# Performance work log

Measured on AMD Instinct MI355X. Metric: run time of the kernel, lower is better.

## Reference

```python
import jax, jax.numpy as jnp
import numpy as np

B, T, C, H = 4, 4096, 1024, 64

def setup_inputs() -> dict:
    key = jax.random.key(0)
    kx, kq, kk, kv = jax.random.split(key, 4)
    # nn.Linear weights are [out, in]; we store them that way and use einsum.
    s = 1.0 / np.sqrt(C)
    return {
        "x": jax.random.normal(kx, (B, T, C), dtype=jnp.float32),
        "Wq": jax.random.uniform(kq, (H, C), dtype=jnp.float32, minval=-s, maxval=s),
        "Wk": jax.random.uniform(kk, (H, C), dtype=jnp.float32, minval=-s, maxval=s),
        "Wv": jax.random.uniform(kv, (H, C), dtype=jnp.float32, minval=-s, maxval=s),
    }

def reference(x, Wq, Wk, Wv):
    # x: [B, T, C]; W*: [H, C] (torch Linear layout)
    Q = jnp.einsum('btc,hc->bth', x, Wq)  # [B, T, H]
    K = jnp.einsum('btc,hc->bth', x, Wk)
    V = jnp.einsum('btc,hc->bth', x, Wv)
    scale = K.shape[-1] ** -0.5
    scores = jnp.einsum('bqh,bkh->bqk', Q, K) * scale  # [B, T, T]
    Tn = x.shape[1]
    causal = jnp.tril(jnp.ones((Tn, Tn), dtype=bool))
    scores = jnp.where(causal, scores, -jnp.inf)
    attn = jax.nn.softmax(scores, axis=-1)
    return jnp.einsum('bqk,bkh->bqh', attn, V)  # [B, T, H]
```

## Files before the change

### kernel.cpp

```cpp
#include <hip/hip_runtime.h>
#include <hip/hip_bf16.h>

#define B_ 4
#define T_ 4096
#define C_ 1024
#define H_ 64

typedef __bf16 bf16x8 __attribute__((ext_vector_type(8)));
typedef float f32x4 __attribute__((ext_vector_type(4)));
typedef unsigned short u16x8 __attribute__((ext_vector_type(8)));

union Frag8 { uint4 u; bf16x8 b; u16x8 s; };

__device__ inline unsigned short bfbits(float f) {
  union { __hip_bfloat16 h; unsigned short u; } cv;
  cv.h = __float2bfloat16(f);
  return cv.u;
}

__device__ inline float b2f(unsigned u) {
  union { unsigned i; float f; } c; c.i = u << 16; return c.f;
}

__device__ inline bf16x8 ldb8(const unsigned short* p) {
  Frag8 f; f.u = *(const uint4*)p; return f.b;
}

__device__ inline unsigned pkbf(float a, float b) {
  union { float f; unsigned u; } ua, ub; ua.f = a; ub.f = b;
  return __builtin_amdgcn_perm(ub.u + 0x8000u, ua.u + 0x8000u, 0x07060302u);
}

__device__ inline Frag8 packA(float4 a0, float4 a1) {
  Frag8 af;
  af.s[0] = bfbits(a0.x); af.s[1] = bfbits(a0.y);
  af.s[2] = bfbits(a0.z); af.s[3] = bfbits(a0.w);
  af.s[4] = bfbits(a1.x); af.s[5] = bfbits(a1.y);
  af.s[6] = bfbits(a1.z); af.s[7] = bfbits(a1.w);
  return af;
}

__device__ inline void gload16(const void* g, void* l) {
  __builtin_amdgcn_global_load_lds(
      (const __attribute__((address_space(1))) unsigned int*)g,
      (__attribute__((address_space(3))) unsigned int*)l, 16, 0, 0);
}

__global__ __launch_bounds__(256) void wconv(const float* __restrict__ Wq,
                                             const float* __restrict__ Wk,
                                             const float* __restrict__ Wv,
                                             unsigned short* __restrict__ Wb) {
  int i = blockIdx.x * 256 + threadIdx.x;
  size_t e = (size_t)i * 4;
  const float* src = (e < 65536) ? (Wq + e)
                   : (e < 131072 ? (Wk + (e - 65536)) : (Wv + (e - 131072)));
  float4 v = *(const float4*)src;
  unsigned long long o =
      (unsigned long long)bfbits(v.x)
    | ((unsigned long long)bfbits(v.y) << 16)
    | ((unsigned long long)bfbits(v.z) << 32)
    | ((unsigned long long)bfbits(v.w) << 48);
  *(unsigned long long*)(Wb + e) = o;
}

__global__ __launch_bounds__(256) void qkv_proj(const float* __restrict__ x,
                                                const unsigned short* __restrict__ Wb,
                                                unsigned short* __restrict__ qkv,
                                                unsigned short* __restrict__ Vt) {
  __shared__ float xs[2][2048];
  __shared__ unsigned short Wsh[2][12288];
  const int lane = threadIdx.x & 63;
  const int wave = threadIdx.x >> 6;
  const int q16 = lane & 15, quad = lane >> 4;
  const int x7 = q16 & 7;
  const size_t row0 = (size_t)blockIdx.x * 32;

  const int sr = lane >> 4;
  const int sc_pos = lane & 15;
  const int rloc = lane >> 3;
  const int cpos = lane & 7;

  f32x4 acc[2][3] = {};

  auto stage = [&](int buf, int kc) {
#pragma unroll
    for (int ii = 0; ii < 2; ++ii) {
      int i = wave * 2 + ii;
      int r = i * 4 + sr;
      int sg = (sc_pos >> 1) ^ (r & 7);
      const float* gp = x + (row0 + r) * C_ + kc + sg * 8 + (sc_pos & 1) * 4;
      gload16(gp, &xs[buf][i * 256]);
    }
#pragma unroll
    for (int jj = 0; jj < 6; ++jj) {
      int j = wave * 6 + jj;
      int g = j * 8 + rloc;
      const unsigned short* gp = Wb + (size_t)(g >> 6) * 65536
                                    + (size_t)(g & 63) * C_ + kc + (cpos ^ rloc) * 8;
      gload16(gp, &Wsh[buf][j * 512]);
    }
  };

  stage(0, 0);
  __syncthreads();

  int cur = 0;
  for (int t = 0; t < 16; ++t) {
    if (t < 15) stage(cur ^ 1, (t + 1) * 64);
    const float* Xc = xs[cur];
    const unsigned short* Wc = Wsh[cur];
#pragma unroll
    for (int s = 0; s < 2; ++s) {
      bf16x8 bf[3];
#pragma unroll
      for (int ct = 0; ct < 3; ++ct) {
        int g = wave * 48 + ct * 16 + q16;
        bf[ct] = ldb8(&Wc[g * 64 + (((s * 4 + quad) ^ x7) * 8)]);
      }
#pragma unroll
      for (int rt = 0; rt < 2; ++rt) {
        int r = rt * 16 + q16;
        int p = ((s * 4 + quad) ^ (r & 7)) * 8;
        const float* ap = &Xc[r * 64 + p];
        float4 a0 = *(const float4*)ap;
        float4 a1 = *(const float4*)(ap + 4);
        Frag8 af = packA(a0, a1);
#pragma unroll
        for (int ct = 0; ct < 3; ++ct)
          acc[rt][ct] = __builtin_amdgcn_mfma_f32_16x16x32_bf16(
              af.b, bf[ct], acc[rt][ct], 0, 0, 0);
      }
    }
    __syncthreads();
    cur ^= 1;
  }

  const int bb = (int)(blockIdx.x >> 7);
#pragma unroll
  for (int rt = 0; rt < 2; ++rt) {
    const int t0 = (int)(row0 - (size_t)bb * T_) + rt * 16 + quad * 4;
#pragma unroll
    for (int ct = 0; ct < 3; ++ct) {
      int gcol = wave * 48 + ct * 16;
      int mat = gcol >> 6, h = (gcol & 63) + q16;
      if (mat == 2) {
        ushort4 v;
        v.x = bfbits(acc[rt][ct][0]); v.y = bfbits(acc[rt][ct][1]);
        v.z = bfbits(acc[rt][ct][2]); v.w = bfbits(acc[rt][ct][3]);
        *(ushort4*)(Vt + ((size_t)bb * H_ + h) * T_ + t0) = v;
      } else {
        float scale = (mat == 0) ? 0.18033688f : 1.0f;
#pragma unroll
        for (int r = 0; r < 4; ++r) {
          size_t row = row0 + rt * 16 + quad * 4 + r;
          qkv[(size_t)mat * 1048576 + row * H_ + h] = bfbits(acc[rt][ct][r] * scale);
        }
      }
    }
  }
}

__global__ __launch_bounds__(256) void attn(const unsigned short* __restrict__ Q,
                                            const unsigned short* __restrict__ K,
                                            const unsigned short* __restrict__ Vt,
                                            float* __restrict__ part,
                                            int lgch, int nslots) {
  const int b = blockIdx.x >> 6;
  const int qblk = 63 - (blockIdx.x & 63);
  const int ki = qblk + 1;
  const int c = blockIdx.y;
  const int cst = c << lgch;
  if (cst >= ki) return;
  const int tcnt = 1 << lgch;
  const int kend = (ki < cst + tcnt) ? ki : cst + tcnt;

  __shared__ unsigned short Ks[2][4096];
  __shared__ unsigned short Vs[2][4096];
  const int lane = threadIdx.x & 63;
  const int wave = threadIdx.x >> 6;
  const int q16 = lane & 15, quad = lane >> 4;
  const int x7 = q16 & 7;
  const int rloc = lane >> 3, cpos = lane & 7;

  const unsigned short* Qb = Q + (size_t)b * T_ * H_;
  const unsigned short* Kb = K + (size_t)b * T_ * H_;
  const unsigned short* Vtb = Vt + (size_t)b * H_ * T_;

  int psi_[2];
#pragma unroll
  for (int ii = 0; ii < 2; ++ii) {
    int g = (wave * 2 + ii) * 8 + rloc;
    psi_[ii] = 8 * ((g & 15) >> 2) + (g & 3) + 4 * ((g >> 4) & 1) + 32 * (g >> 5);
  }

  auto stage = [&](int buf, int kt) {
    const int kkb = kt * 64;
#pragma unroll
    for (int ii = 0; ii < 2; ++ii) {
      int i = wave * 2 + ii;
      gload16(Kb + (size_t)(kkb + psi_[ii]) * H_ + (cpos ^ rloc) * 8,
              &Ks[buf][i * 512]);
      gload16(Vtb + (size_t)(i * 8 + rloc) * T_ + kkb + (cpos ^ rloc) * 8,
              &Vs[buf][i * 512]);
    }
  };

  const int q0w = qblk * 64 + wave * 16;
  bf16x8 qf0 = ldb8(Qb + (size_t)(q0w + q16) * H_ + quad * 8);
  bf16x8 qf1 = ldb8(Qb + (size_t)(q0w + q16) * H_ + 32 + quad * 8);

  f32x4 o[4] = {};
  float m = -3.0e38f, l = 0.0f;
  const int q_abs = q0w + q16;

  stage(0, cst);
  __syncthreads();

  int cur = 0;
  for (int kt = cst; kt < kend; ++kt) {
    const int kkb = kt * 64;
    if (kt + 1 < kend) stage(cur ^ 1, kt + 1);
    const unsigned short* Kc = Ks[cur];
    const unsigned short* Vc = Vs[cur];

    f32x4 st[4];
#pragma unroll
    for (int kb = 0; kb < 4; ++kb) {
      bf16x8 ka0 = ldb8(&Kc[(kb * 16 + q16) * 64 + ((quad ^ x7) * 8)]);
      bf16x8 ka1 = ldb8(&Kc[(kb * 16 + q16) * 64 + (((quad + 4) ^ x7) * 8)]);
      f32x4 s = {0.f, 0.f, 0.f, 0.f};
      s = __builtin_amdgcn_mfma_f32_16x16x32_bf16(ka0, qf0, s, 0, 0, 0);
      s = __builtin_amdgcn_mfma_f32_16x16x32_bf16(ka1, qf1, s, 0, 0, 0);
      st[kb] = s;
    }
    if (kt == ki - 1) {
      const int kb8q = kkb + 8 * quad;
#pragma unroll
      for (int kb = 0; kb < 4; ++kb) {
        const int kof = kb8q + 4 * (kb & 1) + 32 * (kb >> 1);
#pragma unroll
        for (int r = 0; r < 4; ++r)
          if (kof + r > q_abs) st[kb][r] = -3.0e38f;
      }
    }

    float mloc = fmaxf(fmaxf(st[0][0], st[0][1]), fmaxf(st[0][2], st[0][3]));
#pragma unroll
    for (int kb = 1; kb < 4; ++kb)
      mloc = fmaxf(mloc, fmaxf(fmaxf(st[kb][0], st[kb][1]), fmaxf(st[kb][2], st[kb][3])));
    mloc = fmaxf(mloc, __shfl_xor(mloc, 16));
    mloc = fmaxf(mloc, __shfl_xor(mloc, 32));
    const bool defer = __all(mloc - m <= 8.0f);
    const float mnew = defer ? m : fmaxf(m, mloc);
    float lsum = 0.f;
    unsigned pk[4][2];
#pragma unroll
    for (int kb = 0; kb < 4; ++kb) {
      float p0 = exp2f(st[kb][0] - mnew);
      float p1 = exp2f(st[kb][1] - mnew);
      float p2 = exp2f(st[kb][2] - mnew);
      float p3 = exp2f(st[kb][3] - mnew);
      lsum += (p0 + p1) + (p2 + p3);
      pk[kb][0] = pkbf(p0, p1);
      pk[kb][1] = pkbf(p2, p3);
    }
    if (defer) {
      l += lsum;
    } else {
      float alpha = exp2f(m - mnew);
      l = l * alpha + lsum;
      m = mnew;
#pragma unroll
      for (int ct = 0; ct < 4; ++ct) {
        o[ct][0] *= alpha; o[ct][1] *= alpha;
        o[ct][2] *= alpha; o[ct][3] *= alpha;
      }
    }

#pragma unroll
    for (int ks = 0; ks < 2; ++ks) {
      Frag8 pf;
      pf.u.x = pk[2 * ks][0];
      pf.u.y = pk[2 * ks][1];
      pf.u.z = pk[2 * ks + 1][0];
      pf.u.w = pk[2 * ks + 1][1];
      int vp = ((ks * 4 + quad) ^ x7) * 8;
      bf16x8 v0 = ldb8(&Vc[(q16 + 0)  * 64 + vp]);
      bf16x8 v1 = ldb8(&Vc[(q16 + 16) * 64 + vp]);
      bf16x8 v2 = ldb8(&Vc[(q16 + 32) * 64 + vp]);
      bf16x8 v3 = ldb8(&Vc[(q16 + 48) * 64 + vp]);
      o[0] = __builtin_amdgcn_mfma_f32_16x16x32_bf16(v0, pf.b, o[0], 0, 0, 0);
      o[1] = __builtin_amdgcn_mfma_f32_16x16x32_bf16(v1, pf.b, o[1], 0, 0, 0);
      o[2] = __builtin_amdgcn_mfma_f32_16x16x32_bf16(v2, pf.b, o[2], 0, 0, 0);
      o[3] = __builtin_amdgcn_mfma_f32_16x16x32_bf16(v3, pf.b, o[3], 0, 0, 0);
    }
    __syncthreads();
    cur ^= 1;
  }

  const int qtl = qblk * 4 + wave;
  float lr = l;
  lr += __shfl_xor(lr, 16);
  lr += __shfl_xor(lr, 32);
  float* Pf = part + ((size_t)((b << 8) + qtl) * nslots + c) * 544;
  unsigned* Pw = (unsigned*)Pf;
#pragma unroll
  for (int ct = 0; ct < 4; ++ct) {
    uint2 w;
    w.x = pkbf(o[ct][0], o[ct][1]);
    w.y = pkbf(o[ct][2], o[ct][3]);
    *(uint2*)&Pw[(ct * 64 + lane) * 2] = w;
  }
  if (quad == 0) { Pf[512 + q16] = m; Pf[528 + q16] = lr; }
}

__global__ __launch_bounds__(256) void attn_merge(const float* __restrict__ part,
                                                  float* __restrict__ out,
                                                  int lgch, int nslots) {
  const int qt = blockIdx.x;
  const int qtl = qt & 255, b = qt >> 8;
  const int ki = (qtl >> 2) + 1;
  const int nch = (ki + (1 << lgch) - 1) >> lgch;
  const int t = threadIdx.x;
  const int row = t >> 4;
  const int col0 = (t & 15) * 4;
  const int ct = col0 >> 4;
  const int quad_s = (col0 >> 2) & 3;
  const int lane0 = quad_s * 16 + row;
  const float* P0 = part + (size_t)qt * nslots * 544;
  float M = -3.0e38f;
  for (int c2 = 0; c2 < nch; ++c2) M = fmaxf(M, P0[c2 * 544 + 512 + row]);
  float L = 0.f;
  float ax = 0.f, ay = 0.f, az = 0.f, aw = 0.f;
  for (int c2 = 0; c2 < nch; ++c2) {
    const float* P = P0 + c2 * 544;
    float wgt = exp2f(P[512 + row] - M);
    L += wgt * P[528 + row];
    const unsigned* Pww = (const unsigned*)P;
    uint2 wd = *(const uint2*)&Pww[(ct * 64 + lane0) * 2];
    ax += wgt * b2f(wd.x & 0xffffu);
    ay += wgt * b2f(wd.x >> 16);
    az += wgt * b2f(wd.y & 0xffffu);
    aw += wgt * b2f(wd.y >> 16);
  }
  float inv = 1.0f / L;
  float4 r = {ax * inv, ay * inv, az * inv, aw * inv};
  *(float4*)(out + ((size_t)b * T_ + qtl * 16 + row) * H_ + col0) = r;
}

extern "C" void kernel_launch(void* const* d_in, const int* in_sizes, int n_in,
                              void* d_out, int out_size, void* d_ws, size_t ws_size,
                              hipStream_t stream) {
  const float* x  = (const float*)d_in[0];
  const float* Wq = (const float*)d_in[1];
  const float* Wk = (const float*)d_in[2];
  const float* Wv = (const float*)d_in[3];
  float* out = (float*)d_out;
  unsigned short* ws = (unsigned short*)d_ws;

  unsigned short* Wb  = ws;
  unsigned short* qkv = ws + 196608;
  unsigned short* Vt  = qkv + (size_t)2 * 1048576;
  float* part = (float*)(ws + 196608 + (size_t)3 * 1048576);

  const size_t base_bytes = ((size_t)196608 + (size_t)3 * 1048576) * 2;
  const size_t need16 = base_bytes + (size_t)1024 * 16 * 544 * 4;
  int lgch = 3, ny = 8, nslots = 8;
  if (ws_size >= need16) { lgch = 2; ny = 16; nslots = 16; }

  wconv<<<192, 256, 0, stream>>>(Wq, Wk, Wv, Wb);
  qkv_proj<<<512, 256, 0, stream>>>(x, Wb, qkv, Vt);
  attn<<<dim3(256, ny), 256, 0, stream>>>(qkv, qkv + 1048576, Vt, part, lgch, nslots);
  attn_merge<<<1024, 256, 0, stream>>>(part, out, lgch, nslots);
}
```

Before: 161.8 us.

## Widen attention blocks to 128 queries so K/V tiles are shared by eight waves

```diff
diff --git a/kernel.cpp b/kernel.cpp
--- a/kernel.cpp
+++ b/kernel.cpp
@@ -160,19 +160,19 @@
   }
 }
 
-__global__ __launch_bounds__(256) void attn(const unsigned short* __restrict__ Q,
+__global__ __launch_bounds__(512) void attn(const unsigned short* __restrict__ Q,
                                             const unsigned short* __restrict__ K,
                                             const unsigned short* __restrict__ Vt,
                                             float* __restrict__ part,
                                             int lgch, int nslots) {
-  const int b = blockIdx.x >> 6;
-  const int qblk = 63 - (blockIdx.x & 63);
-  const int ki = qblk + 1;
+  const int b = blockIdx.x >> 5;
+  const int qblk = 31 - (blockIdx.x & 31);
+  const int ki_block = 2 * qblk + 2;
   const int c = blockIdx.y;
   const int cst = c << lgch;
-  if (cst >= ki) return;
+  if (cst >= ki_block) return;
   const int tcnt = 1 << lgch;
-  const int kend = (ki < cst + tcnt) ? ki : cst + tcnt;
+  const int kend = (ki_block < cst + tcnt) ? ki_block : cst + tcnt;
 
   __shared__ unsigned short Ks[2][4096];
   __shared__ unsigned short Vs[2][4096];
@@ -186,26 +186,20 @@
   const unsigned short* Kb = K + (size_t)b * T_ * H_;
   const unsigned short* Vtb = Vt + (size_t)b * H_ * T_;
 
-  int psi_[2];
-#pragma unroll
-  for (int ii = 0; ii < 2; ++ii) {
-    int g = (wave * 2 + ii) * 8 + rloc;
-    psi_[ii] = 8 * ((g & 15) >> 2) + (g & 3) + 4 * ((g >> 4) & 1) + 32 * (g >> 5);
-  }
+  const int g_ = wave * 8 + rloc;
+  const int psi_ = 8 * ((g_ & 15) >> 2) + (g_ & 3) + 4 * ((g_ >> 4) & 1)
+                 + 32 * (g_ >> 5);
 
   auto stage = [&](int buf, int kt) {
     const int kkb = kt * 64;
-#pragma unroll
-    for (int ii = 0; ii < 2; ++ii) {
-      int i = wave * 2 + ii;
-      gload16(Kb + (size_t)(kkb + psi_[ii]) * H_ + (cpos ^ rloc) * 8,
-              &Ks[buf][i * 512]);
-      gload16(Vtb + (size_t)(i * 8 + rloc) * T_ + kkb + (cpos ^ rloc) * 8,
-              &Vs[buf][i * 512]);
-    }
+    gload16(Kb + (size_t)(kkb + psi_) * H_ + (cpos ^ rloc) * 8,
+            &Ks[buf][wave * 512]);
+    gload16(Vtb + (size_t)(wave * 8 + rloc) * T_ + kkb + (cpos ^ rloc) * 8,
+            &Vs[buf][wave * 512]);
   };
 
-  const int q0w = qblk * 64 + wave * 16;
+  const int q0w = qblk * 128 + wave * 16;
+  const int kiW = 2 * qblk + (wave >> 2) + 1;
   bf16x8 qf0 = ldb8(Qb + (size_t)(q0w + q16) * H_ + quad * 8);
   bf16x8 qf1 = ldb8(Qb + (size_t)(q0w + q16) * H_ + 32 + quad * 8);
 
@@ -220,98 +214,103 @@
   for (int kt = cst; kt < kend; ++kt) {
     const int kkb = kt * 64;
     if (kt + 1 < kend) stage(cur ^ 1, kt + 1);
-    const unsigned short* Kc = Ks[cur];
-    const unsigned short* Vc = Vs[cur];
-
-    f32x4 st[4];
-#pragma unroll
-    for (int kb = 0; kb < 4; ++kb) {
-      bf16x8 ka0 = ldb8(&Kc[(kb * 16 + q16) * 64 + ((quad ^ x7) * 8)]);
-      bf16x8 ka1 = ldb8(&Kc[(kb * 16 + q16) * 64 + (((quad + 4) ^ x7) * 8)]);
-      f32x4 s = {0.f, 0.f, 0.f, 0.f};
-      s = __builtin_amdgcn_mfma_f32_16x16x32_bf16(ka0, qf0, s, 0, 0, 0);
-      s = __builtin_amdgcn_mfma_f32_16x16x32_bf16(ka1, qf1, s, 0, 0, 0);
-      st[kb] = s;
-    }
-    if (kt == ki - 1) {
-      const int kb8q = kkb + 8 * quad;
+    if (kt < kiW) {
+      const unsigned short* Kc = Ks[cur];
+      const unsigned short* Vc = Vs[cur];
+
+      f32x4 st[4];
 #pragma unroll
       for (int kb = 0; kb < 4; ++kb) {
-        const int kof = kb8q + 4 * (kb & 1) + 32 * (kb >> 1);
-#pragma unroll
-        for (int r = 0; r < 4; ++r)
-          if (kof + r > q_abs) st[kb][r] = -3.0e38f;
-      }
-    }
-
-    float mloc = fmaxf(fmaxf(st[0][0], st[0][1]), fmaxf(st[0][2], st[0][3]));
-#pragma unroll
-    for (int kb = 1; kb < 4; ++kb)
-      mloc = fmaxf(mloc, fmaxf(fmaxf(st[kb][0], st[kb][1]), fmaxf(st[kb][2], st[kb][3])));
-    mloc = fmaxf(mloc, __shfl_xor(mloc, 16));
-    mloc = fmaxf(mloc, __shfl_xor(mloc, 32));
-    const bool defer = __all(mloc - m <= 8.0f);
-    const float mnew = defer ? m : fmaxf(m, mloc);
-    float lsum = 0.f;
-    unsigned pk[4][2];
-#pragma unroll
-    for (int kb = 0; kb < 4; ++kb) {
-      float p0 = exp2f(st[kb][0] - mnew);
-      float p1 = exp2f(st[kb][1] - mnew);
-      float p2 = exp2f(st[kb][2] - mnew);
-      float p3 = exp2f(st[kb][3] - mnew);
-      lsum += (p0 + p1) + (p2 + p3);
-      pk[kb][0] = pkbf(p0, p1);
-      pk[kb][1] = pkbf(p2, p3);
-    }
-    if (defer) {
-      l += lsum;
-    } else {
-      float alpha = exp2f(m - mnew);
-      l = l * alpha + lsum;
-      m = mnew;
-#pragma unroll
-      for (int ct = 0; ct < 4; ++ct) {
-        o[ct][0] *= alpha; o[ct][1] *= alpha;
-        o[ct][2] *= alpha; o[ct][3] *= alpha;
-      }
-    }
-
-#pragma unroll
-    for (int ks = 0; ks < 2; ++ks) {
-      Frag8 pf;
-      pf.u.x = pk[2 * ks][0];
-      pf.u.y = pk[2 * ks][1];
-      pf.u.z = pk[2 * ks + 1][0];
-      pf.u.w = pk[2 * ks + 1][1];
-      int vp = ((ks * 4 + quad) ^ x7) * 8;
-      bf16x8 v0 = ldb8(&Vc[(q16 + 0)  * 64 + vp]);
-      bf16x8 v1 = ldb8(&Vc[(q16 + 16) * 64 + vp]);
-      bf16x8 v2 = ldb8(&Vc[(q16 + 32) * 64 + vp]);
-      bf16x8 v3 = ldb8(&Vc[(q16 + 48) * 64 + vp]);
-      o[0] = __builtin_amdgcn_mfma_f32_16x16x32_bf16(v0, pf.b, o[0], 0, 0, 0);
-      o[1] = __builtin_amdgcn_mfma_f32_16x16x32_bf16(v1, pf.b, o[1], 0, 0, 0);
-      o[2] = __builtin_amdgcn_mfma_f32_16x16x32_bf16(v2, pf.b, o[2], 0, 0, 0);
-      o[3] = __builtin_amdgcn_mfma_f32_16x16x32_bf16(v3, pf.b, o[3], 0, 0, 0);
+        bf16x8 ka0 = ldb8(&Kc[(kb * 16 + q16) * 64 + ((quad ^ x7) * 8)]);
+        bf16x8 ka1 = ldb8(&Kc[(kb * 16 + q16) * 64 + (((quad + 4) ^ x7) * 8)]);
+        f32x4 s = {0.f, 0.f, 0.f, 0.f};
+        s = __builtin_amdgcn_mfma_f32_16x16x32_bf16(ka0, qf0, s, 0, 0, 0);
+        s = __builtin_amdgcn_mfma_f32_16x16x32_bf16(ka1, qf1, s, 0, 0, 0);
+        st[kb] = s;
+      }
+      if (kt == kiW - 1) {
+        const int kb8q = kkb + 8 * quad;
+#pragma unroll
+        for (int kb = 0; kb < 4; ++kb) {
+          const int kof = kb8q + 4 * (kb & 1) + 32 * (kb >> 1);
+#pragma unroll
+          for (int r = 0; r < 4; ++r)
+            if (kof + r > q_abs) st[kb][r] = -3.0e38f;
+        }
+      }
+
+      float mloc = fmaxf(fmaxf(st[0][0], st[0][1]), fmaxf(st[0][2], st[0][3]));
+#pragma unroll
+      for (int kb = 1; kb < 4; ++kb)
+        mloc = fmaxf(mloc, fmaxf(fmaxf(st[kb][0], st[kb][1]),
+                                 fmaxf(st[kb][2], st[kb][3])));
+      mloc = fmaxf(mloc, __shfl_xor(mloc, 16));
+      mloc = fmaxf(mloc, __shfl_xor(mloc, 32));
+      const bool defer = __all(mloc - m <= 8.0f);
+      const float mnew = defer ? m : fmaxf(m, mloc);
+      float lsum = 0.f;
+      unsigned pk[4][2];
+#pragma unroll
+      for (int kb = 0; kb < 4; ++kb) {
+        float p0 = exp2f(st[kb][0] - mnew);
+        float p1 = exp2f(st[kb][1] - mnew);
+        float p2 = exp2f(st[kb][2] - mnew);
+        float p3 = exp2f(st[kb][3] - mnew);
+        lsum += (p0 + p1) + (p2 + p3);
+        pk[kb][0] = pkbf(p0, p1);
+        pk[kb][1] = pkbf(p2, p3);
+      }
+      if (defer) {
+        l += lsum;
+      } else {
+        float alpha = exp2f(m - mnew);
+        l = l * alpha + lsum;
+        m = mnew;
+#pragma unroll
+        for (int ct = 0; ct < 4; ++ct) {
+          o[ct][0] *= alpha; o[ct][1] *= alpha;
+          o[ct][2] *= alpha; o[ct][3] *= alpha;
+        }
+      }
+
+#pragma unroll
+      for (int ks = 0; ks < 2; ++ks) {
+        Frag8 pf;
+        pf.u.x = pk[2 * ks][0];
+        pf.u.y = pk[2 * ks][1];
+        pf.u.z = pk[2 * ks + 1][0];
+        pf.u.w = pk[2 * ks + 1][1];
+        int vp = ((ks * 4 + quad) ^ x7) * 8;
+        bf16x8 v0 = ldb8(&Vc[(q16 + 0)  * 64 + vp]);
+        bf16x8 v1 = ldb8(&Vc[(q16 + 16) * 64 + vp]);
+        bf16x8 v2 = ldb8(&Vc[(q16 + 32) * 64 + vp]);
+        bf16x8 v3 = ldb8(&Vc[(q16 + 48) * 64 + vp]);
+        o[0] = __builtin_amdgcn_mfma_f32_16x16x32_bf16(v0, pf.b, o[0], 0, 0, 0);
+        o[1] = __builtin_amdgcn_mfma_f32_16x16x32_bf16(v1, pf.b, o[1], 0, 0, 0);
+        o[2] = __builtin_amdgcn_mfma_f32_16x16x32_bf16(v2, pf.b, o[2], 0, 0, 0);
+        o[3] = __builtin_amdgcn_mfma_f32_16x16x32_bf16(v3, pf.b, o[3], 0, 0, 0);
+      }
     }
     __syncthreads();
     cur ^= 1;
   }
 
-  const int qtl = qblk * 4 + wave;
-  float lr = l;
-  lr += __shfl_xor(lr, 16);
-  lr += __shfl_xor(lr, 32);
-  float* Pf = part + ((size_t)((b << 8) + qtl) * nslots + c) * 544;
-  unsigned* Pw = (unsigned*)Pf;
-#pragma unroll
-  for (int ct = 0; ct < 4; ++ct) {
-    uint2 w;
-    w.x = pkbf(o[ct][0], o[ct][1]);
-    w.y = pkbf(o[ct][2], o[ct][3]);
-    *(uint2*)&Pw[(ct * 64 + lane) * 2] = w;
-  }
-  if (quad == 0) { Pf[512 + q16] = m; Pf[528 + q16] = lr; }
+  if (cst < kiW) {
+    const int qtl = qblk * 8 + wave;
+    float lr = l;
+    lr += __shfl_xor(lr, 16);
+    lr += __shfl_xor(lr, 32);
+    float* Pf = part + ((size_t)((b << 8) + qtl) * nslots + c) * 544;
+    unsigned* Pw = (unsigned*)Pf;
+#pragma unroll
+    for (int ct = 0; ct < 4; ++ct) {
+      uint2 w;
+      w.x = pkbf(o[ct][0], o[ct][1]);
+      w.y = pkbf(o[ct][2], o[ct][3]);
+      *(uint2*)&Pw[(ct * 64 + lane) * 2] = w;
+    }
+    if (quad == 0) { Pf[512 + q16] = m; Pf[528 + q16] = lr; }
+  }
 }
 
 __global__ __launch_bounds__(256) void attn_merge(const float* __restrict__ part,
@@ -370,6 +369,6 @@
 
   wconv<<<192, 256, 0, stream>>>(Wq, Wk, Wv, Wb);
   qkv_proj<<<512, 256, 0, stream>>>(x, Wb, qkv, Vt);
-  attn<<<dim3(256, ny), 256, 0, stream>>>(qkv, qkv + 1048576, Vt, part, lgch, nslots);
+  attn<<<dim3(128, ny), 512, 0, stream>>>(qkv, qkv + 1048576, Vt, part, lgch, nslots);
   attn_merge<<<1024, 256, 0, stream>>>(part, out, lgch, nslots);
 }
```

Result: slower. 168.6 us (+4.1%).

## Load K and V fragments directly from global memory, dropping LDS staging

Applied to the files above, without the earlier changes.

```diff
diff --git a/kernel.cpp b/kernel.cpp
--- a/kernel.cpp
+++ b/kernel.cpp
@@ -166,71 +166,59 @@
                                             float* __restrict__ part,
                                             int lgch, int nslots) {
   const int b = blockIdx.x >> 6;
-  const int qblk = 63 - (blockIdx.x & 63);
-  const int ki = qblk + 1;
+  const int g = 63 - (blockIdx.x & 63);
+  const int ki = g + 1;
   const int c = blockIdx.y;
   const int cst = c << lgch;
   if (cst >= ki) return;
   const int tcnt = 1 << lgch;
   const int kend = (ki < cst + tcnt) ? ki : cst + tcnt;
 
-  __shared__ unsigned short Ks[2][4096];
-  __shared__ unsigned short Vs[2][4096];
   const int lane = threadIdx.x & 63;
   const int wave = threadIdx.x >> 6;
   const int q16 = lane & 15, quad = lane >> 4;
-  const int x7 = q16 & 7;
-  const int rloc = lane >> 3, cpos = lane & 7;
 
   const unsigned short* Qb = Q + (size_t)b * T_ * H_;
   const unsigned short* Kb = K + (size_t)b * T_ * H_;
   const unsigned short* Vtb = Vt + (size_t)b * H_ * T_;
 
-  int psi_[2];
-#pragma unroll
-  for (int ii = 0; ii < 2; ++ii) {
-    int g = (wave * 2 + ii) * 8 + rloc;
-    psi_[ii] = 8 * ((g & 15) >> 2) + (g & 3) + 4 * ((g >> 4) & 1) + 32 * (g >> 5);
-  }
-
-  auto stage = [&](int buf, int kt) {
-    const int kkb = kt * 64;
-#pragma unroll
-    for (int ii = 0; ii < 2; ++ii) {
-      int i = wave * 2 + ii;
-      gload16(Kb + (size_t)(kkb + psi_[ii]) * H_ + (cpos ^ rloc) * 8,
-              &Ks[buf][i * 512]);
-      gload16(Vtb + (size_t)(i * 8 + rloc) * T_ + kkb + (cpos ^ rloc) * 8,
-              &Vs[buf][i * 512]);
-    }
-  };
-
-  const int q0w = qblk * 64 + wave * 16;
-  bf16x8 qf0 = ldb8(Qb + (size_t)(q0w + q16) * H_ + quad * 8);
-  bf16x8 qf1 = ldb8(Qb + (size_t)(q0w + q16) * H_ + 32 + quad * 8);
+  const int qtl = g * 4 + wave;
+  const int q_abs = qtl * 16 + q16;
+
+  const int kbase = 8 * (q16 >> 2) + (q16 & 3);
+
+  bf16x8 qf0 = ldb8(Qb + (size_t)(qtl * 16 + q16) * H_ + quad * 8);
+  bf16x8 qf1 = ldb8(Qb + (size_t)(qtl * 16 + q16) * H_ + 32 + quad * 8);
 
   f32x4 o[4] = {};
   float m = -3.0e38f, l = 0.0f;
-  const int q_abs = q0w + q16;
-
-  stage(0, cst);
-  __syncthreads();
-
-  int cur = 0;
+
   for (int kt = cst; kt < kend; ++kt) {
     const int kkb = kt * 64;
-    if (kt + 1 < kend) stage(cur ^ 1, kt + 1);
-    const unsigned short* Kc = Ks[cur];
-    const unsigned short* Vc = Vs[cur];
+
+    const unsigned short* Ktile = Kb + (size_t)kkb * H_ + quad * 8;
+    bf16x8 ka[4][2];
+#pragma unroll
+    for (int kb = 0; kb < 4; ++kb) {
+      const unsigned short* kr =
+          Ktile + (size_t)(kbase + 4 * (kb & 1) + 32 * (kb >> 1)) * H_;
+      ka[kb][0] = ldb8(kr);
+      ka[kb][1] = ldb8(kr + 32);
+    }
+    const unsigned short* Vtile = Vtb + kkb + quad * 8;
+    bf16x8 vf[2][4];
+#pragma unroll
+    for (int ks = 0; ks < 2; ++ks)
+#pragma unroll
+      for (int ct = 0; ct < 4; ++ct)
+        vf[ks][ct] = ldb8(Vtile + (size_t)(q16 + 16 * ct) * T_ + ks * 32);
 
     f32x4 st[4];
 #pragma unroll
     for (int kb = 0; kb < 4; ++kb) {
-      bf16x8 ka0 = ldb8(&Kc[(kb * 16 + q16) * 64 + ((quad ^ x7) * 8)]);
-      bf16x8 ka1 = ldb8(&Kc[(kb * 16 + q16) * 64 + (((quad + 4) ^ x7) * 8)]);
       f32x4 s = {0.f, 0.f, 0.f, 0.f};
-      s = __builtin_amdgcn_mfma_f32_16x16x32_bf16(ka0, qf0, s, 0, 0, 0);
-      s = __builtin_amdgcn_mfma_f32_16x16x32_bf16(ka1, qf1, s, 0, 0, 0);
+      s = __builtin_amdgcn_mfma_f32_16x16x32_bf16(ka[kb][0], qf0, s, 0, 0, 0);
+      s = __builtin_amdgcn_mfma_f32_16x16x32_bf16(ka[kb][1], qf1, s, 0, 0, 0);
       st[kb] = s;
     }
     if (kt == ki - 1) {
@@ -247,7 +235,8 @@
     float mloc = fmaxf(fmaxf(st[0][0], st[0][1]), fmaxf(st[0][2], st[0][3]));
 #pragma unroll
     for (int kb = 1; kb < 4; ++kb)
-      mloc = fmaxf(mloc, fmaxf(fmaxf(st[kb][0], st[kb][1]), fmaxf(st[kb][2], st[kb][3])));
+      mloc = fmaxf(mloc, fmaxf(fmaxf(st[kb][0], st[kb][1]),
+                               fmaxf(st[kb][2], st[kb][3])));
     mloc = fmaxf(mloc, __shfl_xor(mloc, 16));
     mloc = fmaxf(mloc, __shfl_xor(mloc, 32));
     const bool defer = __all(mloc - m <= 8.0f);
@@ -284,21 +273,13 @@
       pf.u.y = pk[2 * ks][1];
       pf.u.z = pk[2 * ks + 1][0];
       pf.u.w = pk[2 * ks + 1][1];
-      int vp = ((ks * 4 + quad) ^ x7) * 8;
-      bf16x8 v0 = ldb8(&Vc[(q16 + 0)  * 64 + vp]);
-      bf16x8 v1 = ldb8(&Vc[(q16 + 16) * 64 + vp]);
-      bf16x8 v2 = ldb8(&Vc[(q16 + 32) * 64 + vp]);
-      bf16x8 v3 = ldb8(&Vc[(q16 + 48) * 64 + vp]);
-      o[0] = __builtin_amdgcn_mfma_f32_16x16x32_bf16(v0, pf.b, o[0], 0, 0, 0);
-      o[1] = __builtin_amdgcn_mfma_f32_16x16x32_bf16(v1, pf.b, o[1], 0, 0, 0);
-      o[2] = __builtin_amdgcn_mfma_f32_16x16x32_bf16(v2, pf.b, o[2], 0, 0, 0);
-      o[3] = __builtin_amdgcn_mfma_f32_16x16x32_bf16(v3, pf.b, o[3], 0, 0, 0);
-    }
-    __syncthreads();
-    cur ^= 1;
-  }
-
-  const int qtl = qblk * 4 + wave;
+      o[0] = __builtin_amdgcn_mfma_f32_16x16x32_bf16(vf[ks][0], pf.b, o[0], 0, 0, 0);
+      o[1] = __builtin_amdgcn_mfma_f32_16x16x32_bf16(vf[ks][1], pf.b, o[1], 0, 0, 0);
+      o[2] = __builtin_amdgcn_mfma_f32_16x16x32_bf16(vf[ks][2], pf.b, o[2], 0, 0, 0);
+      o[3] = __builtin_amdgcn_mfma_f32_16x16x32_bf16(vf[ks][3], pf.b, o[3], 0, 0, 0);
+    }
+  }
+
   float lr = l;
   lr += __shfl_xor(lr, 16);
   lr += __shfl_xor(lr, 32);
```

Measured after the change: 218.9 us. 1.35x slower.

## Split QKV projection across matrices per block and raise MFMA wave priority

Applied to the files above, without the earlier changes.

```diff
diff --git a/kernel.cpp b/kernel.cpp
--- a/kernel.cpp
+++ b/kernel.cpp
@@ -68,19 +68,23 @@
                                                 unsigned short* __restrict__ qkv,
                                                 unsigned short* __restrict__ Vt) {
   __shared__ float xs[2][2048];
-  __shared__ unsigned short Wsh[2][12288];
+  __shared__ unsigned short Wsh[2][4096];
   const int lane = threadIdx.x & 63;
   const int wave = threadIdx.x >> 6;
   const int q16 = lane & 15, quad = lane >> 4;
   const int x7 = q16 & 7;
-  const size_t row0 = (size_t)blockIdx.x * 32;
+  const int mat  = (int)(blockIdx.x % 3);
+  const int rblk = (int)(blockIdx.x / 3);
+  const size_t row0 = (size_t)rblk * 32;
 
   const int sr = lane >> 4;
   const int sc_pos = lane & 15;
   const int rloc = lane >> 3;
   const int cpos = lane & 7;
 
-  f32x4 acc[2][3] = {};
+  const unsigned short* Wm = Wb + (size_t)mat * 65536;
+
+  f32x4 acc[2] = {};
 
   auto stage = [&](int buf, int kc) {
 #pragma unroll
@@ -92,11 +96,10 @@
       gload16(gp, &xs[buf][i * 256]);
     }
 #pragma unroll
-    for (int jj = 0; jj < 6; ++jj) {
-      int j = wave * 6 + jj;
+    for (int jj = 0; jj < 2; ++jj) {
+      int j = wave * 2 + jj;
       int g = j * 8 + rloc;
-      const unsigned short* gp = Wb + (size_t)(g >> 6) * 65536
-                                    + (size_t)(g & 63) * C_ + kc + (cpos ^ rloc) * 8;
+      const unsigned short* gp = Wm + (size_t)g * C_ + kc + (cpos ^ rloc) * 8;
       gload16(gp, &Wsh[buf][j * 512]);
     }
   };
@@ -111,12 +114,8 @@
     const unsigned short* Wc = Wsh[cur];
 #pragma unroll
     for (int s = 0; s < 2; ++s) {
-      bf16x8 bf[3];
-#pragma unroll
-      for (int ct = 0; ct < 3; ++ct) {
-        int g = wave * 48 + ct * 16 + q16;
-        bf[ct] = ldb8(&Wc[g * 64 + (((s * 4 + quad) ^ x7) * 8)]);
-      }
+      int g = wave * 16 + q16;
+      bf16x8 bf = ldb8(&Wc[g * 64 + (((s * 4 + quad) ^ x7) * 8)]);
 #pragma unroll
       for (int rt = 0; rt < 2; ++rt) {
         int r = rt * 16 + q16;
@@ -125,36 +124,30 @@
         float4 a0 = *(const float4*)ap;
         float4 a1 = *(const float4*)(ap + 4);
         Frag8 af = packA(a0, a1);
-#pragma unroll
-        for (int ct = 0; ct < 3; ++ct)
-          acc[rt][ct] = __builtin_amdgcn_mfma_f32_16x16x32_bf16(
-              af.b, bf[ct], acc[rt][ct], 0, 0, 0);
+        acc[rt] = __builtin_amdgcn_mfma_f32_16x16x32_bf16(
+            af.b, bf, acc[rt], 0, 0, 0);
       }
     }
     __syncthreads();
     cur ^= 1;
   }
 
-  const int bb = (int)(blockIdx.x >> 7);
+  const int bb = rblk >> 7;
+  const int h = wave * 16 + q16;
 #pragma unroll
   for (int rt = 0; rt < 2; ++rt) {
     const int t0 = (int)(row0 - (size_t)bb * T_) + rt * 16 + quad * 4;
-#pragma unroll
-    for (int ct = 0; ct < 3; ++ct) {
-      int gcol = wave * 48 + ct * 16;
-      int mat = gcol >> 6, h = (gcol & 63) + q16;
-      if (mat == 2) {
-        ushort4 v;
-        v.x = bfbits(acc[rt][ct][0]); v.y = bfbits(acc[rt][ct][1]);
-        v.z = bfbits(acc[rt][ct][2]); v.w = bfbits(acc[rt][ct][3]);
-        *(ushort4*)(Vt + ((size_t)bb * H_ + h) * T_ + t0) = v;
-      } else {
-        float scale = (mat == 0) ? 0.18033688f : 1.0f;
-#pragma unroll
-        for (int r = 0; r < 4; ++r) {
-          size_t row = row0 + rt * 16 + quad * 4 + r;
-          qkv[(size_t)mat * 1048576 + row * H_ + h] = bfbits(acc[rt][ct][r] * scale);
-        }
+    if (mat == 2) {
+      ushort4 v;
+      v.x = bfbits(acc[rt][0]); v.y = bfbits(acc[rt][1]);
+      v.z = bfbits(acc[rt][2]); v.w = bfbits(acc[rt][3]);
+      *(ushort4*)(Vt + ((size_t)bb * H_ + h) * T_ + t0) = v;
+    } else {
+      float scale = (mat == 0) ? 0.18033688f : 1.0f;
+#pragma unroll
+      for (int r = 0; r < 4; ++r) {
+        size_t row = row0 + rt * 16 + quad * 4 + r;
+        qkv[(size_t)mat * 1048576 + row * H_ + h] = bfbits(acc[rt][r] * scale);
       }
     }
   }
@@ -224,6 +217,7 @@
     const unsigned short* Vc = Vs[cur];
 
     f32x4 st[4];
+    __builtin_amdgcn_s_setprio(1);
 #pragma unroll
     for (int kb = 0; kb < 4; ++kb) {
       bf16x8 ka0 = ldb8(&Kc[(kb * 16 + q16) * 64 + ((quad ^ x7) * 8)]);
@@ -233,6 +227,7 @@
       s = __builtin_amdgcn_mfma_f32_16x16x32_bf16(ka1, qf1, s, 0, 0, 0);
       st[kb] = s;
     }
+    __builtin_amdgcn_s_setprio(0);
     if (kt == ki - 1) {
       const int kb8q = kkb + 8 * quad;
 #pragma unroll
@@ -247,7 +242,8 @@
     float mloc = fmaxf(fmaxf(st[0][0], st[0][1]), fmaxf(st[0][2], st[0][3]));
 #pragma unroll
     for (int kb = 1; kb < 4; ++kb)
-      mloc = fmaxf(mloc, fmaxf(fmaxf(st[kb][0], st[kb][1]), fmaxf(st[kb][2], st[kb][3])));
+      mloc = fmaxf(mloc, fmaxf(fmaxf(st[kb][0], st[kb][1]),
+                               fmaxf(st[kb][2], st[kb][3])));
     mloc = fmaxf(mloc, __shfl_xor(mloc, 16));
     mloc = fmaxf(mloc, __shfl_xor(mloc, 32));
     const bool defer = __all(mloc - m <= 8.0f);
@@ -277,6 +273,7 @@
       }
     }
 
+    __builtin_amdgcn_s_setprio(1);
 #pragma unroll
     for (int ks = 0; ks < 2; ++ks) {
       Frag8 pf;
@@ -294,6 +291,7 @@
       o[2] = __builtin_amdgcn_mfma_f32_16x16x32_bf16(v2, pf.b, o[2], 0, 0, 0);
       o[3] = __builtin_amdgcn_mfma_f32_16x16x32_bf16(v3, pf.b, o[3], 0, 0, 0);
     }
+    __builtin_amdgcn_s_setprio(0);
     __syncthreads();
     cur ^= 1;
   }
@@ -369,7 +367,7 @@
   if (ws_size >= need16) { lgch = 2; ny = 16; nslots = 16; }
 
   wconv<<<192, 256, 0, stream>>>(Wq, Wk, Wv, Wb);
-  qkv_proj<<<512, 256, 0, stream>>>(x, Wb, qkv, Vt);
+  qkv_proj<<<1536, 256, 0, stream>>>(x, Wb, qkv, Vt);
   attn<<<dim3(256, ny), 256, 0, stream>>>(qkv, qkv + 1048576, Vt, part, lgch, nslots);
   attn_merge<<<1024, 256, 0, stream>>>(part, out, lgch, nslots);
 }
```

Result: slower. 199.0 us (+22.9%).
